# Kernel tuning notes

Hardware: AMD Instinct MI355X
Metric: run time of the kernel (lower is better)

The kernel has to match this reference:

```python
import jax, jax.numpy as jnp
import numpy as np

GRID = 9          # 9x9 taxi grid -> 81 zones
N_ZONES = GRID * GRID
OBS_DIM = 48      # obs[:, :48] used by every zone's dense layer
MAX_ADJ = 5       # self + up/down/left/right
BATCH = 32768
NEG_INF = -1e9


def _grid_adjacency():
    """Padded adjacency (self + valid 4-neighbors) for a 9x9 grid."""
    idx = np.zeros((N_ZONES, MAX_ADJ), dtype=np.int32)
    mask = np.zeros((N_ZONES, MAX_ADJ), dtype=np.float32)
    for i in range(N_ZONES):
        r, c = divmod(i, GRID)
        nbrs = [i]
        if r > 0: nbrs.append(i - GRID)
        if r < GRID - 1: nbrs.append(i + GRID)
        if c > 0: nbrs.append(i - 1)
        if c < GRID - 1: nbrs.append(i + 1)
        for j, n in enumerate(nbrs):
            idx[i, j] = n
            mask[i, j] = 1.0
    return idx, mask


def setup_inputs() -> dict:
    key = jax.random.key(0)
    k_obs, k_w = jax.random.split(key)
    obs = jax.random.normal(k_obs, (BATCH, OBS_DIM), dtype=jnp.float32)
    # per-zone dense weights [48 -> adjacent_num], padded to MAX_ADJ
    W = jax.random.normal(k_w, (N_ZONES, OBS_DIM, MAX_ADJ), dtype=jnp.float32) * 0.1
    b = jnp.zeros((N_ZONES, MAX_ADJ), dtype=jnp.float32)
    idx_np, mask_np = _grid_adjacency()
    return {"obs": obs, "W": W, "b": b,
            "idx": jnp.asarray(idx_np), "mask": jnp.asarray(mask_np)}


def reference(obs, W, b, idx, mask):
    x = obs[:, :OBS_DIM]                              # [B, 48]
    # batched tiny GEMMs: one [48 -> K] dense per zone
    logits = jnp.einsum('bd,ndk->bnk', x, W) + b      # [B, N, K]
    logits = jnp.where(mask > 0, logits, NEG_INF)     # padded slots -> 0 after softmax
    probs = jax.nn.softmax(logits, axis=-1) * mask    # [B, N, K]
    B = obs.shape[0]
    n, k = idx.shape
    rows = jnp.broadcast_to(jnp.arange(n)[:, None], (n, k))  # zone index per slot
    out = jnp.zeros((B, n, N_ZONES), dtype=obs.dtype)
    # scatter each zone's softmax probs into its adjacency positions of an 81-vector
    out = out.at[:, rows, idx].add(probs)
    return out                                        # [B, 81, 81]
```

## Files before the change

### kernel.cpp

```cpp
#include <hip/hip_runtime.h>

#define NZ 81
#define OBS_DIM 48
#define MAX_ADJ 5
#define NTASK (NZ * MAX_ADJ)
#define NEG_INF -1000000000.0f
#define BLOCK 512
#define ROWS 16

__global__ __launch_bounds__(BLOCK) void taxi_actor_kernel(
    const float* __restrict__ obs,
    const float* __restrict__ W,
    const float* __restrict__ bias,
    const int*   __restrict__ idx,
    const float* __restrict__ mask,
    float* __restrict__ out)
{
    __shared__ float s_obs[ROWS * OBS_DIM];
    __shared__ float s_logits[NTASK];
    __shared__ int   s_idx[NTASK];
    __shared__ float s_tile[NZ * NZ];

    const int tid = threadIdx.x;
    const size_t b0 = (size_t)blockIdx.x * ROWS;

    for (int i = tid; i < ROWS * OBS_DIM; i += BLOCK)
        s_obs[i] = obs[b0 * OBS_DIM + i];
    for (int i = tid; i < NZ * NZ; i += BLOCK)
        s_tile[i] = 0.0f;

    float w[OBS_DIM];
    float bia = 0.0f;
    if (tid < NTASK) {
        const int n = tid / MAX_ADJ;
        const int k = tid - n * MAX_ADJ;
        const float* __restrict__ Wp = W + (size_t)n * (OBS_DIM * MAX_ADJ) + k;
        #pragma unroll
        for (int d = 0; d < OBS_DIM; ++d) w[d] = Wp[d * MAX_ADJ];
        bia = bias[tid];
        s_idx[tid] = (mask[tid] > 0.0f) ? idx[tid] : -1;
    }
    __syncthreads();

    for (int r = 0; r < ROWS; ++r) {
        float acc = bia;
        if (tid < NTASK) {
            const float* __restrict__ o = s_obs + r * OBS_DIM;
            #pragma unroll
            for (int d = 0; d < OBS_DIM; ++d)
                acc = fmaf(o[d], w[d], acc);
        }
        __syncthreads();
        if (tid < NTASK)
            s_logits[tid] = (s_idx[tid] >= 0) ? acc : NEG_INF;
        __syncthreads();
        if (tid < NZ) {
            float l[MAX_ADJ], p[MAX_ADJ];
            float m = NEG_INF;
            #pragma unroll
            for (int k = 0; k < MAX_ADJ; ++k) {
                l[k] = s_logits[tid * MAX_ADJ + k];
                m = fmaxf(m, l[k]);
            }
            float s = 0.0f;
            #pragma unroll
            for (int k = 0; k < MAX_ADJ; ++k) {
                p[k] = __expf(l[k] - m);
                s += p[k];
            }
            const float inv = 1.0f / s;
            #pragma unroll
            for (int k = 0; k < MAX_ADJ; ++k) {
                const int z = s_idx[tid * MAX_ADJ + k];
                if (z >= 0) s_tile[tid * NZ + z] = p[k] * inv;
            }
        }
        __syncthreads();
        float* __restrict__ outb = out + (b0 + r) * (size_t)(NZ * NZ);
        for (int i = tid; i < NZ * NZ; i += BLOCK)
            outb[i] = s_tile[i];
    }
}

extern "C" void kernel_launch(void* const* d_in, const int* in_sizes, int n_in,
                              void* d_out, int out_size, void* d_ws, size_t ws_size,
                              hipStream_t stream) {
    const float* obs  = (const float*)d_in[0];
    const float* W    = (const float*)d_in[1];
    const float* bias = (const float*)d_in[2];
    const int*   idx  = (const int*)d_in[3];
    const float* mask = (const float*)d_in[4];
    float* out = (float*)d_out;

    const int B = in_sizes[0] / OBS_DIM;
    taxi_actor_kernel<<<B / ROWS, BLOCK, 0, stream>>>(obs, W, bias, idx, mask, out);
}
```

Measured before the change: 177.1 us.

## Batch all rows per block phase and write output via precomputed gather map

Replaces the per-row compute/softmax/tile loop, which needed three barriers per row, with three block-wide phases. All 16 rows' logits are computed at once with float4 shared-memory reads, softmax runs in parallel over rows×zones, and output is written through a per-thread precomputed position-to-slot map. This drops the dense shared-memory tile and most synchronisation. The cost is higher register pressure from the 16 accumulators and the 13-entry map, and the output remains a large streaming write.

Measured after the change: 268.6 us. +51.7%, slower.

```diff
diff --git a/kernel.cpp b/kernel.cpp
--- a/kernel.cpp
+++ b/kernel.cpp
@@ -4,9 +4,11 @@
 #define OBS_DIM 48
 #define MAX_ADJ 5
 #define NTASK (NZ * MAX_ADJ)
+#define TPAD 408
 #define NEG_INF -1000000000.0f
 #define BLOCK 512
 #define ROWS 16
+#define NPOS 13
 
 __global__ __launch_bounds__(BLOCK) void taxi_actor_kernel(
     const float* __restrict__ obs,
@@ -17,68 +19,93 @@
     float* __restrict__ out)
 {
     __shared__ float s_obs[ROWS * OBS_DIM];
-    __shared__ float s_logits[NTASK];
+    __shared__ float s_lp[ROWS][TPAD];
     __shared__ int   s_idx[NTASK];
-    __shared__ float s_tile[NZ * NZ];
 
     const int tid = threadIdx.x;
     const size_t b0 = (size_t)blockIdx.x * ROWS;
 
     for (int i = tid; i < ROWS * OBS_DIM; i += BLOCK)
         s_obs[i] = obs[b0 * OBS_DIM + i];
-    for (int i = tid; i < NZ * NZ; i += BLOCK)
-        s_tile[i] = 0.0f;
+    if (tid < NTASK)
+        s_idx[tid] = (mask[tid] > 0.0f) ? idx[tid] : -1;
+    __syncthreads();
 
-    float w[OBS_DIM];
-    float bia = 0.0f;
+    int tmap[NPOS];
+    #pragma unroll
+    for (int i = 0; i < NPOS; ++i) {
+        tmap[i] = -1;
+        const int p = tid + i * BLOCK;
+        if (p < NZ * NZ) {
+            const int n = p / NZ;
+            const int z = p - n * NZ;
+            #pragma unroll
+            for (int k = 0; k < MAX_ADJ; ++k)
+                if (s_idx[n * MAX_ADJ + k] == z) tmap[i] = n * MAX_ADJ + k;
+        }
+    }
+
     if (tid < NTASK) {
+        float acc[ROWS];
+        #pragma unroll
+        for (int r = 0; r < ROWS; ++r) acc[r] = 0.0f;
         const int n = tid / MAX_ADJ;
         const int k = tid - n * MAX_ADJ;
-        const float* __restrict__ Wp = W + (size_t)n * (OBS_DIM * MAX_ADJ) + k;
+        const float* __restrict__ Wp = W + n * (OBS_DIM * MAX_ADJ) + k;
         #pragma unroll
-        for (int d = 0; d < OBS_DIM; ++d) w[d] = Wp[d * MAX_ADJ];
-        bia = bias[tid];
-        s_idx[tid] = (mask[tid] > 0.0f) ? idx[tid] : -1;
+        for (int d4 = 0; d4 < OBS_DIM; d4 += 4) {
+            const float w0 = Wp[(d4 + 0) * MAX_ADJ];
+            const float w1 = Wp[(d4 + 1) * MAX_ADJ];
+            const float w2 = Wp[(d4 + 2) * MAX_ADJ];
+            const float w3 = Wp[(d4 + 3) * MAX_ADJ];
+            #pragma unroll
+            for (int r = 0; r < ROWS; ++r) {
+                const float4 o = *reinterpret_cast<const float4*>(&s_obs[r * OBS_DIM + d4]);
+                acc[r] = fmaf(o.x, w0, acc[r]);
+                acc[r] = fmaf(o.y, w1, acc[r]);
+                acc[r] = fmaf(o.z, w2, acc[r]);
+                acc[r] = fmaf(o.w, w3, acc[r]);
+            }
+        }
+        const float bv = bias[tid];
+        const bool valid = (s_idx[tid] >= 0);
+        #pragma unroll
+        for (int r = 0; r < ROWS; ++r)
+            s_lp[r][tid] = valid ? (acc[r] + bv) : NEG_INF;
+    }
+    __syncthreads();
+
+    for (int j = tid; j < ROWS * NZ; j += BLOCK) {
+        const int r = j / NZ;
+        const int n = j - r * NZ;
+        float l[MAX_ADJ];
+        float m = NEG_INF;
+        #pragma unroll
+        for (int k = 0; k < MAX_ADJ; ++k) {
+            l[k] = s_lp[r][n * MAX_ADJ + k];
+            m = fmaxf(m, l[k]);
+        }
+        float ssum = 0.0f;
+        #pragma unroll
+        for (int k = 0; k < MAX_ADJ; ++k) {
+            l[k] = __expf(l[k] - m);
+            ssum += l[k];
+        }
+        const float inv = 1.0f / ssum;
+        #pragma unroll
+        for (int k = 0; k < MAX_ADJ; ++k)
+            s_lp[r][n * MAX_ADJ + k] = l[k] * inv;
     }
     __syncthreads();
 
     for (int r = 0; r < ROWS; ++r) {
-        float acc = bia;
-        if (tid < NTASK) {
-            const float* __restrict__ o = s_obs + r * OBS_DIM;
-            #pragma unroll
-            for (int d = 0; d < OBS_DIM; ++d)
-                acc = fmaf(o[d], w[d], acc);
+        float* __restrict__ ob = out + (b0 + r) * (size_t)(NZ * NZ);
+        #pragma unroll
+        for (int i = 0; i < NPOS; ++i) {
+            const int p = tid + i * BLOCK;
+            if (p < NZ * NZ)
+                ob[p] = (tmap[i] >= 0) ? s_lp[r][tmap[i]] : 0.0f;
         }
-        __syncthreads();
-        if (tid < NTASK)
-            s_logits[tid] = (s_idx[tid] >= 0) ? acc : NEG_INF;
-        __syncthreads();
-        if (tid < NZ) {
-            float l[MAX_ADJ], p[MAX_ADJ];
-            float m = NEG_INF;
-            #pragma unroll
-            for (int k = 0; k < MAX_ADJ; ++k) {
-                l[k] = s_logits[tid * MAX_ADJ + k];
-                m = fmaxf(m, l[k]);
-            }
-            float s = 0.0f;
-            #pragma unroll
-            for (int k = 0; k < MAX_ADJ; ++k) {
-                p[k] = __expf(l[k] - m);
-                s += p[k];
-            }
-            const float inv = 1.0f / s;
-            #pragma unroll
-            for (int k = 0; k < MAX_ADJ; ++k) {
-                const int z = s_idx[tid * MAX_ADJ + k];
-                if (z >= 0) s_tile[tid * NZ + z] = p[k] * inv;
-            }
-        }
-        __syncthreads();
-        float* __restrict__ outb = out + (b0 + r) * (size_t)(NZ * NZ);
-        for (int i = tid; i < NZ * NZ; i += BLOCK)
-            outb[i] = s_tile[i];
     }
 }
 
```
